# Kernel tuning notes

Measured on AMD Instinct MI355X. Metric: run time of the kernel, lower is better.

Reference implementation:

```python
import jax, jax.numpy as jnp
import numpy as np

B, S, D = 1, 2048, 2048
H, KVH, HD = 16, 8, 128
ROPE_THETA = 1e6
P_POW, C_SHIFT = 8, 7.0
MASK_VAL = -7.0  # = -c so masked bpmax base ~ scores only (finite under ^8)


def rotate_half(x):
    x1, x2 = jnp.split(x, 2, axis=-1)
    return jnp.concatenate([-x2, x1], axis=-1)


def setup_inputs() -> dict:
    key = jax.random.key(0)
    ks = jax.random.split(key, 10)
    hidden_states = jax.random.normal(ks[0], (B, S, D), dtype=jnp.float32)
    # RoPE tables (Qwen3-style, theta=1e6)
    inv_freq = 1.0 / (ROPE_THETA ** (jnp.arange(0, HD, 2, dtype=jnp.float32) / HD))
    freqs = jnp.arange(S, dtype=jnp.float32)[:, None] * inv_freq[None, :]
    emb = jnp.concatenate([freqs, freqs], axis=-1)  # [S, HD]
    cos = jnp.broadcast_to(jnp.cos(emb)[None], (B, S, HD)).astype(jnp.float32)
    sin = jnp.broadcast_to(jnp.sin(emb)[None], (B, S, HD)).astype(jnp.float32)
    sc = D ** -0.5
    q_proj_w = jax.random.normal(ks[1], (D, H * HD), dtype=jnp.float32) * sc
    k_proj_w = jax.random.normal(ks[2], (D, KVH * HD), dtype=jnp.float32) * sc
    v_proj_w = jax.random.normal(ks[3], (D, KVH * HD), dtype=jnp.float32) * sc
    o_proj_w = jax.random.normal(ks[4], (H * HD, D), dtype=jnp.float32) * (H * HD) ** -0.5
    q_norm_w = jnp.ones((HD,), dtype=jnp.float32)
    k_norm_w = jnp.ones((HD,), dtype=jnp.float32)
    # Stored RMSNorm denominators (rsqrt-like buffers from training), ~O(1)
    q_denom = 0.5 + jax.random.uniform(ks[5], (B, S, H, 1), dtype=jnp.float32)
    k_denom = 0.5 + jax.random.uniform(ks[6], (B, S, KVH, 1), dtype=jnp.float32)
    # Stored bpmax normalizer buffer rd (per-head, per-query-row)
    rd = 5.0 + 10.0 * jax.random.uniform(ks[7], (1, H, S, 1), dtype=jnp.float32)
    # Causal mask with MASK_VAL for masked positions (finite under bpmax)
    causal = jnp.tril(jnp.ones((S, S), dtype=bool))
    attention_mask = jnp.where(causal, 0.0, MASK_VAL)[None, None].astype(jnp.float32)
    return {
        'hidden_states': hidden_states, 'cos': cos, 'sin': sin,
        'q_proj_w': q_proj_w, 'k_proj_w': k_proj_w, 'v_proj_w': v_proj_w,
        'o_proj_w': o_proj_w, 'q_norm_w': q_norm_w, 'k_norm_w': k_norm_w,
        'q_denom': q_denom, 'k_denom': k_denom, 'rd': rd,
        'attention_mask': attention_mask,
    }


def reference(hidden_states, cos, sin, q_proj_w, k_proj_w, v_proj_w, o_proj_w,
              q_norm_w, k_norm_w, q_denom, k_denom, rd, attention_mask):
    b, s, d = hidden_states.shape
    hd = q_norm_w.shape[0]
    scaling = hd ** -0.5
    # Projections + per-head RMSNorm (eval path: stored denominator buffer)
    q = (hidden_states @ q_proj_w).reshape(b, s, -1, hd)
    q = (q_norm_w * (q * q_denom[:, :s])).transpose(0, 2, 1, 3)   # [B,H,S,hd]
    k = (hidden_states @ k_proj_w).reshape(b, s, -1, hd)
    k = (k_norm_w * (k * k_denom[:, :s])).transpose(0, 2, 1, 3)   # [B,KVH,S,hd]
    v = (hidden_states @ v_proj_w).reshape(b, s, -1, hd).transpose(0, 2, 1, 3)
    # RoPE
    cos_ = cos[:, None, :, :]
    sin_ = sin[:, None, :, :]
    q = q * cos_ + rotate_half(q) * sin_
    k = k * cos_ + rotate_half(k) * sin_
    # GQA: repeat kv heads
    groups = q.shape[1] // k.shape[1]
    k = jnp.repeat(k, groups, axis=1)
    v = jnp.repeat(v, groups, axis=1)
    # Scores + mask + bpmax power-law normalization (eval path)
    aw = jnp.einsum('bhqd,bhkd->bhqk', q, k) * scaling
    aw = aw + attention_mask[:, :, :, :s]
    aw = ((aw + C_SHIFT) / rd[:, :, :s, :]) ** P_POW
    # Attention output + output projection
    out = jnp.einsum('bhqk,bhkd->bhqd', aw, v)
    out = out.transpose(0, 2, 1, 3).reshape(b, s, -1)
    return out @ o_proj_w
```

## Files before the change

### kernel.cpp

```cpp
#include <hip/hip_runtime.h>
#include <cstdint>
#include <cstddef>


namespace {
constexpr int kS = 2048;
constexpr int kD = 2048;
constexpr int kH = 16;
constexpr int kKVH = 8;
constexpr int kHD = 128;
constexpr float kScale = 0.08838834764831845f;
constexpr size_t MB = 1u << 20;
}

using f32x4 = __attribute__((ext_vector_type(4))) float;
using bfrag = __attribute__((ext_vector_type(8))) short;
using float4v = __attribute__((ext_vector_type(4))) float;
using short4v = __attribute__((ext_vector_type(4))) short;

__device__ __forceinline__ unsigned short f2b(float f) {
  union { float f; unsigned u; } x; x.f = f;
  unsigned r = x.u + 0x7FFFu + ((x.u >> 16) & 1u);
  return (unsigned short)(r >> 16);
}

__device__ __forceinline__ float b2f(unsigned short u) {
  union { unsigned u; float f; } x; x.u = ((unsigned)u) << 16;
  return x.f;
}

__device__ __forceinline__ void gload_lds16(const void* g, void* l) {
  __builtin_amdgcn_global_load_lds(
      (const __attribute__((address_space(1))) unsigned*)g,
      (__attribute__((address_space(3))) unsigned*)l, 16, 0, 0);
}

__global__ __launch_bounds__(256) void qwen_cast_bf16(const float* __restrict__ in,
                                                      unsigned short* __restrict__ out,
                                                      int n4) {
  int i = blockIdx.x * 256 + threadIdx.x;
  if (i >= n4) return;
  float4v v = *(const float4v*)(in + (size_t)i * 4);
  short4v o;
  o[0] = (short)f2b(v[0]); o[1] = (short)f2b(v[1]);
  o[2] = (short)f2b(v[2]); o[3] = (short)f2b(v[3]);
  int i4 = i * 4;
  int row = i4 >> 11, col = i4 & 2047;
  int scol = col ^ ((row & 3) << 3);
  *(short4v*)(out + ((size_t)row << 11) + scol) = o;
}

__global__ __launch_bounds__(256) void qwen_tw(const float* __restrict__ in, int R, int C,
                                               unsigned short* __restrict__ out, int ldo) {
  __shared__ float t[64][65];
  int c0 = blockIdx.x * 64, r0 = blockIdx.y * 64;
  int tr = threadIdx.x >> 6, tc = threadIdx.x & 63;
#pragma unroll
  for (int p = 0; p < 16; ++p) {
    int i = p * 4 + tr;
    t[i][tc] = in[(size_t)(r0 + i) * C + c0 + tc];
  }
  __syncthreads();
#pragma unroll
  for (int p = 0; p < 16; ++p) {
    int i = p * 4 + tr;
    int orow = c0 + i;
    int ocol = r0 + tc;
    int scol = ocol ^ ((orow & 3) << 3);
    out[(size_t)orow * ldo + scol] = f2b(t[tc][i]);
  }
}

template <int BM, bool BF16OUT>
__global__ __launch_bounds__(256) void qwen_gemm_bt(const unsigned short* __restrict__ A,
                                                    const unsigned short* __restrict__ Bt,
                                                    void* __restrict__ Cv,
                                                    int M, int N, int K) {
  __shared__ unsigned short As[2][BM * 32];
  __shared__ unsigned short Bs[2][128 * 32];
  constexpr int MR = BM / 32;
  const int nwg = gridDim.x * gridDim.y;
  int lin = blockIdx.y * gridDim.x + blockIdx.x;
  if ((nwg & 7) == 0) { int qq = nwg >> 3; lin = (lin & 7) * qq + (lin >> 3); }
  const int bxx = lin % gridDim.x, byy = lin / gridDim.x;
  const int tid = threadIdx.x, lane = tid & 63, w = tid >> 6;
  const int wr = w >> 1, wc = w & 1;
  const int row0 = bxx * BM, col0 = byy * 128;
  f32x4 acc[MR][4] = {};
  const int koff = (lane >> 4) << 3;
  const int swz = (lane & 3) << 3;
  const int kread = koff ^ swz;
  const int rA = wr * (BM / 2) + (lane & 15);
  const int rB = wc * 64 + (lane & 15);

  auto stage = [&](int kt, int b) {
#pragma unroll
    for (int c = 0; c < BM / 64; ++c) {
      int off = (c * 256 + tid) * 16;
      int e = off >> 1;
      int r = e >> 5, cc = e & 31;
      gload_lds16(A + (size_t)(row0 + r) * K + kt + cc, (char*)(&As[b][0]) + off);
    }
#pragma unroll
    for (int c = 0; c < 2; ++c) {
      int off = (c * 256 + tid) * 16;
      int e = off >> 1;
      int r = e >> 5, cc = e & 31;
      gload_lds16(Bt + (size_t)(col0 + r) * K + kt + cc, (char*)(&Bs[b][0]) + off);
    }
  };

  const int nk = K >> 5;
  stage(0, 0);
  asm volatile("s_waitcnt vmcnt(0)" ::: "memory");
  __builtin_amdgcn_s_barrier();
  int buf = 0;
#pragma unroll 1
  for (int t = 0; t < nk; ++t) {
    if (t + 1 < nk) stage((t + 1) << 5, buf ^ 1);
    bfrag aF[MR], bF[4];
#pragma unroll
    for (int m = 0; m < MR; ++m)
      aF[m] = *(const bfrag*)(&As[buf][0] + (rA + m * 16) * 32 + kread);
#pragma unroll
    for (int n = 0; n < 4; ++n)
      bF[n] = *(const bfrag*)(&Bs[buf][0] + (rB + n * 16) * 32 + kread);
#pragma unroll
    for (int m = 0; m < MR; ++m)
#pragma unroll
      for (int n = 0; n < 4; ++n)
        acc[m][n] = __builtin_amdgcn_mfma_f32_16x16x32_bf16(aF[m], bF[n], acc[m][n], 0, 0, 0);
    asm volatile("s_waitcnt vmcnt(0)" ::: "memory");
    __builtin_amdgcn_s_barrier();
    buf ^= 1;
  }
  const int cr = (lane >> 4) << 2;
  const int cc2 = lane & 15;
#pragma unroll
  for (int m = 0; m < MR; ++m)
#pragma unroll
    for (int n = 0; n < 4; ++n) {
      int r = row0 + wr * (BM / 2) + m * 16 + cr;
      int c = col0 + wc * 64 + n * 16 + cc2;
#pragma unroll
      for (int j = 0; j < 4; ++j) {
        if constexpr (BF16OUT) {
          ((unsigned short*)Cv)[(size_t)(r + j) * N + c] = f2b(acc[m][n][j]);
        } else {
          ((float*)Cv)[(size_t)(r + j) * N + c] = acc[m][n][j];
        }
      }
    }
}

__global__ __launch_bounds__(256) void qwen_rope(const unsigned short* __restrict__ Cq16,
                                                 const float* __restrict__ cosb,
                                                 const float* __restrict__ sinb,
                                                 const float* __restrict__ qnw,
                                                 const float* __restrict__ knw,
                                                 const float* __restrict__ qden,
                                                 const float* __restrict__ kden,
                                                 unsigned short* __restrict__ Qb,
                                                 unsigned short* __restrict__ Kswz) {
  __shared__ unsigned short SMrow[4096];
  const int s = blockIdx.x;
  const int t = threadIdx.x;
  {
    const char* src = (const char*)(Cq16 + (size_t)s * 4096);
    gload_lds16(src + t * 16, (char*)SMrow + t * 16);
    gload_lds16(src + 4096 + t * 16, (char*)SMrow + 4096 + t * 16);
  }
  __syncthreads();
  const float* cs = cosb + (size_t)s * kHD;
  const float* sn = sinb + (size_t)s * kHD;
#pragma unroll
  for (int rep = 0; rep < 8; ++rep) {
    int idx = rep * 256 + t;
    int h = idx >> 7, d = idx & 127;
    float dn = qden[s * kH + h];
    float v = b2f(SMrow[idx]) * dn * qnw[d];
    float pv = b2f(SMrow[(h << 7) + (d ^ 64)]) * dn * qnw[d ^ 64];
    float rot = (d < 64) ? -pv : pv;
    Qb[((size_t)h * kS + s) * kHD + d] = f2b(v * cs[d] + rot * sn[d]);
  }
  const int kt = s >> 6, key = s & 63;
#pragma unroll
  for (int rep = 0; rep < 4; ++rep) {
    int idx = rep * 256 + t;
    int h = idx >> 7, d = idx & 127;
    float dn = kden[s * kKVH + h];
    float v = b2f(SMrow[2048 + idx]) * dn * knw[d];
    float pv = b2f(SMrow[2048 + (h << 7) + (d ^ 64)]) * dn * knw[d ^ 64];
    float rot = (d < 64) ? -pv : pv;
    size_t rowi = ((size_t)(h * 32 + kt) * 64 + key) * 128;
    Kswz[rowi + (d ^ ((key & 7) << 3))] = f2b(v * cs[d] + rot * sn[d]);
  }
}

__global__ __launch_bounds__(256) void qwen_vtr(const unsigned short* __restrict__ Cq16,
                                                unsigned short* __restrict__ Vswz) {
  __shared__ unsigned short t[64][66];
  int kvh = blockIdx.x, st = blockIdx.y, dt = blockIdx.z;
  int s0 = st * 64, d0 = dt * 64;
  int tr = threadIdx.x >> 6, tc = threadIdx.x & 63;
#pragma unroll
  for (int p = 0; p < 16; ++p) {
    int i = p * 4 + tr;
    t[i][tc] = Cq16[(size_t)(s0 + i) * 4096 + 3072 + (kvh << 7) + d0 + tc];
  }
  __syncthreads();
#pragma unroll
  for (int p = 0; p < 16; ++p) {
    int i = p * 4 + tr;
    int d = d0 + i;
    size_t rowi = ((size_t)(kvh * 32 + st) * 128 + d) * 64;
    Vswz[rowi + (tc ^ ((d & 15) << 2))] = t[tc][i];
  }
}

#define STAGE8(cc, bb)                                                 \
  do {                                                                 \
    const char* ks_ = Ksrc + ((size_t)(cc) << 14) + tid * 16;          \
    const char* vs_ = Vsrc + ((size_t)(cc) << 14) + tid * 16;          \
    char* kd_ = (char*)(&KV[bb][0]) + tid * 16;                        \
    char* vd_ = (char*)(&KV[2 + (bb)][0]) + tid * 16;                  \
    _Pragma("unroll") for (int it = 0; it < 4; ++it) {                 \
      gload_lds16(ks_ + it * 4096, kd_ + it * 4096);                   \
      gload_lds16(vs_ + it * 4096, vd_ + it * 4096);                   \
    }                                                                  \
  } while (0)

__global__ __launch_bounds__(256, 2) void qwen_attn(const unsigned short* __restrict__ Qb,
                                                    const unsigned short* __restrict__ Kswz,
                                                    const unsigned short* __restrict__ Vswz,
                                                    const float* __restrict__ rd,
                                                    unsigned short* __restrict__ AO) {
  __shared__ unsigned short KV[4][8192];
  const int bid = blockIdx.x;
  const int kvh = bid & 7;
  const int u = (bid >> 3) & 31;
  const int v = bid >> 8;
  const int h = kvh * 2 + (u & 1);
  const int j = u >> 1;
  const int qt = v ? j : (31 - j);
  const int q0 = qt * 64;
  const int nch = qt + 1;
  const int tid = threadIdx.x, lane = tid & 63, w = tid >> 6;
  const int l15 = lane & 15, g = lane >> 4;
  const int qw0 = q0 + w * 16;
  const int qlim = qw0 + l15;
  const int swzK = (l15 & 7) << 3;
  const int swzV = l15 << 2;

  bfrag qF[4];
#pragma unroll
  for (int dc = 0; dc < 4; ++dc)
    qF[dc] = *(const bfrag*)(Qb + ((size_t)h * kS + qw0 + l15) * kHD + dc * 32 + g * 8);
  const float inv = 1.0f / rd[(size_t)h * kS + qw0 + l15];

  const char* Ksrc = (const char*)Kswz + ((size_t)(kvh * 32) << 14);
  const char* Vsrc = (const char*)Vswz + ((size_t)(kvh * 32) << 14);

  f32x4 outa[8] = {};

  STAGE8(0, 0);
#pragma unroll 1
  for (int c = 0; c < nch; ++c) {
    const int b = c & 1;
    asm volatile("s_waitcnt vmcnt(0)" ::: "memory");
    __builtin_amdgcn_s_barrier();
    if (c + 1 < nch) STAGE8(c + 1, b ^ 1);
    __builtin_amdgcn_s_setprio(1);
    const unsigned short* Kbuf = &KV[b][0];
    const unsigned short* Vbuf = &KV[2 + b][0];
    f32x4 sc[4] = {};
#pragma unroll
    for (int t = 0; t < 4; ++t) {
      const unsigned short* kr = Kbuf + (t * 16 + l15) * 128;
#pragma unroll
      for (int dc = 0; dc < 4; ++dc) {
        bfrag kf = *(const bfrag*)(kr + ((dc * 32 + g * 8) ^ swzK));
        sc[t] = __builtin_amdgcn_mfma_f32_16x16x32_bf16(kf, qF[dc], sc[t], 0, 0, 0);
      }
    }
    const int kbase = c * 64;
    const bool full = (c < qt);
    union { bfrag f; unsigned u[4]; } pb[2];
#pragma unroll
    for (int t = 0; t < 4; ++t) {
      unsigned short bb[4];
#pragma unroll
      for (int rr = 0; rr < 4; ++rr) {
        float tt = sc[t][rr] * kScale;
        int key = kbase + t * 16 + g * 4 + rr;
        tt += (full || key <= qlim) ? 7.0f : 0.0f;
        float y = tt * inv;
        float y2 = y * y, y4 = y2 * y2;
        bb[rr] = f2b(y4 * y4);
      }
      pb[t >> 1].u[(t & 1) * 2 + 0] = (unsigned)bb[0] | ((unsigned)bb[1] << 16);
      pb[t >> 1].u[(t & 1) * 2 + 1] = (unsigned)bb[2] | ((unsigned)bb[3] << 16);
    }
#pragma unroll
    for (int dt = 0; dt < 8; ++dt) {
      const unsigned short* vr = Vbuf + (dt * 16 + l15) * 64;
#pragma unroll
      for (int pr = 0; pr < 2; ++pr) {
        union { bfrag f; short4v h4[2]; } va;
        va.h4[0] = *(const short4v*)(vr + ((pr * 32 + g * 4) ^ swzV));
        va.h4[1] = *(const short4v*)(vr + ((pr * 32 + 16 + g * 4) ^ swzV));
        outa[dt] = __builtin_amdgcn_mfma_f32_16x16x32_bf16(va.f, pb[pr].f, outa[dt], 0, 0, 0);
      }
    }
    __builtin_amdgcn_s_setprio(0);
  }
  {
    const int swzA = (l15 & 3) << 3;
#pragma unroll
    for (int dt = 0; dt < 8; ++dt) {
      short4v o;
      o[0] = (short)f2b(outa[dt][0]); o[1] = (short)f2b(outa[dt][1]);
      o[2] = (short)f2b(outa[dt][2]); o[3] = (short)f2b(outa[dt][3]);
      int col = h * 128 + dt * 16 + g * 4;
      *(short4v*)(AO + (size_t)(qw0 + l15) * kD + (col ^ swzA)) = o;
    }
  }
}

extern "C" void kernel_launch(void* const* d_in, const int* in_sizes, int n_in,
                              void* d_out, int out_size, void* d_ws, size_t ws_size,
                              hipStream_t stream) {
  (void)in_sizes; (void)n_in; (void)out_size; (void)ws_size;
  const float* hidden = (const float*)d_in[0];
  const float* cosb   = (const float*)d_in[1];
  const float* sinb   = (const float*)d_in[2];
  const float* qw     = (const float*)d_in[3];
  const float* kw     = (const float*)d_in[4];
  const float* vw     = (const float*)d_in[5];
  const float* ow     = (const float*)d_in[6];
  const float* qnw    = (const float*)d_in[7];
  const float* knw    = (const float*)d_in[8];
  const float* qden   = (const float*)d_in[9];
  const float* kden   = (const float*)d_in[10];
  const float* rd     = (const float*)d_in[11];
  float* out = (float*)d_out;

  char* ws = (char*)d_ws;
  unsigned short* hsb  = (unsigned short*)(ws + 0 * MB);
  unsigned short* Wt   = (unsigned short*)(ws + 8 * MB);
  unsigned short* Cq16 = (unsigned short*)(ws + 24 * MB);
  unsigned short* Qb   = (unsigned short*)(ws + 56 * MB);
  unsigned short* Kswz = (unsigned short*)(ws + 64 * MB);
  unsigned short* Vswz = (unsigned short*)(ws + 68 * MB);
  unsigned short* AO   = (unsigned short*)(ws + 72 * MB);
  unsigned short* Ot   = (unsigned short*)(ws + 80 * MB);

  qwen_cast_bf16<<<4096, 256, 0, stream>>>(hidden, hsb, 2048 * 2048 / 4);
  qwen_tw<<<dim3(32, 32), 256, 0, stream>>>(qw, 2048, 2048, Wt, 2048);
  qwen_tw<<<dim3(16, 32), 256, 0, stream>>>(kw, 2048, 1024, Wt + (size_t)2048 * 2048, 2048);
  qwen_tw<<<dim3(16, 32), 256, 0, stream>>>(vw, 2048, 1024, Wt + (size_t)3072 * 2048, 2048);
  qwen_tw<<<dim3(32, 32), 256, 0, stream>>>(ow, 2048, 2048, Ot, 2048);
  qwen_gemm_bt<128, true><<<dim3(16, 32), 256, 0, stream>>>(hsb, Wt, Cq16, 2048, 4096, 2048);
  qwen_rope<<<2048, 256, 0, stream>>>(Cq16, cosb, sinb, qnw, knw, qden, kden, Qb, Kswz);
  qwen_vtr<<<dim3(8, 32, 2), 256, 0, stream>>>(Cq16, Vswz);
  qwen_attn<<<512, 256, 0, stream>>>(Qb, Kswz, Vswz, rd, AO);
  qwen_gemm_bt<128, false><<<dim3(16, 16), 256, 0, stream>>>(AO, Ot, out, 2048, 2048, 2048);
}
```

Baseline: 168.4 us.

## Split attention over key chunks by parity with 128-row query tiles and reduction

```diff
diff --git a/kernel.cpp b/kernel.cpp
--- a/kernel.cpp
+++ b/kernel.cpp
@@ -234,72 +234,87 @@
                                                     const unsigned short* __restrict__ Kswz,
                                                     const unsigned short* __restrict__ Vswz,
                                                     const float* __restrict__ rd,
-                                                    unsigned short* __restrict__ AO) {
+                                                    float* __restrict__ Pacc) {
   __shared__ unsigned short KV[4][8192];
   const int bid = blockIdx.x;
   const int kvh = bid & 7;
-  const int u = (bid >> 3) & 31;
-  const int v = bid >> 8;
-  const int h = kvh * 2 + (u & 1);
-  const int j = u >> 1;
-  const int qt = v ? j : (31 - j);
-  const int q0 = qt * 64;
-  const int nch = qt + 1;
+  const int x = bid >> 3;
+  const int half = x >> 5;
+  const int x5 = x & 31;
+  const int hb = x5 >> 4;
+  const int t0 = x5 & 15;
+  const int qt = half ? t0 : (15 - t0);
+  const int parity = half;
+  const int h = kvh * 2 + hb;
+  const int q0 = qt * 128;
+  const int nlc = qt + 1;
   const int tid = threadIdx.x, lane = tid & 63, w = tid >> 6;
   const int l15 = lane & 15, g = lane >> 4;
-  const int qw0 = q0 + w * 16;
-  const int qlim = qw0 + l15;
+  const int qw0 = q0 + w * 32;
+  const int qlim0 = qw0 + l15;
+  const int qlim1 = qw0 + 16 + l15;
   const int swzK = (l15 & 7) << 3;
   const int swzV = l15 << 2;
 
-  bfrag qF[4];
-#pragma unroll
-  for (int dc = 0; dc < 4; ++dc)
-    qF[dc] = *(const bfrag*)(Qb + ((size_t)h * kS + qw0 + l15) * kHD + dc * 32 + g * 8);
-  const float inv = 1.0f / rd[(size_t)h * kS + qw0 + l15];
+  bfrag qF[2][4];
+#pragma unroll
+  for (int qs = 0; qs < 2; ++qs)
+#pragma unroll
+    for (int dc = 0; dc < 4; ++dc)
+      qF[qs][dc] = *(const bfrag*)(Qb + ((size_t)h * kS + qw0 + qs * 16 + l15) * kHD +
+                                   dc * 32 + g * 8);
+  const float inv[2] = {1.0f / rd[(size_t)h * kS + qlim0],
+                        1.0f / rd[(size_t)h * kS + qlim1]};
 
   const char* Ksrc = (const char*)Kswz + ((size_t)(kvh * 32) << 14);
   const char* Vsrc = (const char*)Vswz + ((size_t)(kvh * 32) << 14);
 
-  f32x4 outa[8] = {};
-
-  STAGE8(0, 0);
+  f32x4 outa[2][8] = {};
+
+  STAGE8(parity, 0);
 #pragma unroll 1
-  for (int c = 0; c < nch; ++c) {
-    const int b = c & 1;
+  for (int lc = 0; lc < nlc; ++lc) {
+    const int c = parity + 2 * lc;
+    const int b = lc & 1;
     asm volatile("s_waitcnt vmcnt(0)" ::: "memory");
     __builtin_amdgcn_s_barrier();
-    if (c + 1 < nch) STAGE8(c + 1, b ^ 1);
+    if (lc + 1 < nlc) STAGE8(c + 2, b ^ 1);
     __builtin_amdgcn_s_setprio(1);
     const unsigned short* Kbuf = &KV[b][0];
     const unsigned short* Vbuf = &KV[2 + b][0];
-    f32x4 sc[4] = {};
-#pragma unroll
-    for (int t = 0; t < 4; ++t) {
-      const unsigned short* kr = Kbuf + (t * 16 + l15) * 128;
+    f32x4 sc[2][4] = {};
+#pragma unroll
+    for (int t4 = 0; t4 < 4; ++t4) {
+      const unsigned short* kr = Kbuf + (t4 * 16 + l15) * 128;
 #pragma unroll
       for (int dc = 0; dc < 4; ++dc) {
         bfrag kf = *(const bfrag*)(kr + ((dc * 32 + g * 8) ^ swzK));
-        sc[t] = __builtin_amdgcn_mfma_f32_16x16x32_bf16(kf, qF[dc], sc[t], 0, 0, 0);
+        sc[0][t4] = __builtin_amdgcn_mfma_f32_16x16x32_bf16(kf, qF[0][dc], sc[0][t4], 0, 0, 0);
+        sc[1][t4] = __builtin_amdgcn_mfma_f32_16x16x32_bf16(kf, qF[1][dc], sc[1][t4], 0, 0, 0);
       }
     }
     const int kbase = c * 64;
-    const bool full = (c < qt);
-    union { bfrag f; unsigned u[4]; } pb[2];
-#pragma unroll
-    for (int t = 0; t < 4; ++t) {
-      unsigned short bb[4];
-#pragma unroll
-      for (int rr = 0; rr < 4; ++rr) {
-        float tt = sc[t][rr] * kScale;
-        int key = kbase + t * 16 + g * 4 + rr;
-        tt += (full || key <= qlim) ? 7.0f : 0.0f;
-        float y = tt * inv;
-        float y2 = y * y, y4 = y2 * y2;
-        bb[rr] = f2b(y4 * y4);
+    const bool full = (kbase + 63 <= qw0);
+    union { bfrag f; unsigned u[4]; } pb[2][2];
+#pragma unroll
+    for (int qs = 0; qs < 2; ++qs) {
+      const int ql = qs ? qlim1 : qlim0;
+      const float iv = inv[qs];
+#pragma unroll
+      for (int t4 = 0; t4 < 4; ++t4) {
+        unsigned short bb[4];
+#pragma unroll
+        for (int rr = 0; rr < 4; ++rr) {
+          float tt = sc[qs][t4][rr] * kScale;
+          int key = kbase + t4 * 16 + g * 4 + rr;
+          tt += (full || key <= ql) ? 7.0f : 0.0f;
+          float y = tt * iv;
+          float y2 = y * y, y4 = y2 * y2;
+          bb[rr] = f2b(y4 * y4);
+        }
+        pb[qs][t4 >> 1].u[(t4 & 1) * 2 + 0] = (unsigned)bb[0] | ((unsigned)bb[1] << 16);
+        pb[qs][t4 >> 1].u[(t4 & 1) * 2 + 1] = (unsigned)bb[2] | ((unsigned)bb[3] << 16);
       }
-      pb[t >> 1].u[(t & 1) * 2 + 0] = (unsigned)bb[0] | ((unsigned)bb[1] << 16);
-      pb[t >> 1].u[(t & 1) * 2 + 1] = (unsigned)bb[2] | ((unsigned)bb[3] << 16);
     }
 #pragma unroll
     for (int dt = 0; dt < 8; ++dt) {
@@ -309,21 +324,45 @@
         union { bfrag f; short4v h4[2]; } va;
         va.h4[0] = *(const short4v*)(vr + ((pr * 32 + g * 4) ^ swzV));
         va.h4[1] = *(const short4v*)(vr + ((pr * 32 + 16 + g * 4) ^ swzV));
-        outa[dt] = __builtin_amdgcn_mfma_f32_16x16x32_bf16(va.f, pb[pr].f, outa[dt], 0, 0, 0);
+        outa[0][dt] = __builtin_amdgcn_mfma_f32_16x16x32_bf16(va.f, pb[0][pr].f, outa[0][dt], 0, 0, 0);
+        outa[1][dt] = __builtin_amdgcn_mfma_f32_16x16x32_bf16(va.f, pb[1][pr].f, outa[1][dt], 0, 0, 0);
       }
     }
     __builtin_amdgcn_s_setprio(0);
   }
   {
-    const int swzA = (l15 & 3) << 3;
-#pragma unroll
-    for (int dt = 0; dt < 8; ++dt) {
-      short4v o;
-      o[0] = (short)f2b(outa[dt][0]); o[1] = (short)f2b(outa[dt][1]);
-      o[2] = (short)f2b(outa[dt][2]); o[3] = (short)f2b(outa[dt][3]);
-      int col = h * 128 + dt * 16 + g * 4;
-      *(short4v*)(AO + (size_t)(qw0 + l15) * kD + (col ^ swzA)) = o;
-    }
+    float* Po = Pacc + (((size_t)(h * 16 + qt) * 2 + parity) << 14);
+#pragma unroll
+    for (int qs = 0; qs < 2; ++qs) {
+      const int qrow = w * 32 + qs * 16 + l15;
+#pragma unroll
+      for (int dt = 0; dt < 8; ++dt) {
+        f32x4 v = outa[qs][dt];
+        *(f32x4*)(Po + qrow * 128 + dt * 16 + g * 4) = v;
+      }
+    }
+  }
+}
+
+__global__ __launch_bounds__(256) void qwen_ared(const float* __restrict__ Pacc,
+                                                 unsigned short* __restrict__ AO) {
+  const int unit = blockIdx.x;
+  const int h = unit >> 4, qt = unit & 15;
+  const float* P0 = Pacc + ((size_t)unit << 15);
+  const float* P1 = P0 + 16384;
+  const int t = threadIdx.x;
+#pragma unroll
+  for (int i = 0; i < 16; ++i) {
+    int idx = (i * 256 + t) * 4;
+    f32x4 a = *(const f32x4*)(P0 + idx);
+    f32x4 b = *(const f32x4*)(P1 + idx);
+    int qrow = idx >> 7, d = idx & 127;
+    int q = qt * 128 + qrow;
+    int col = h * 128 + d;
+    short4v o;
+    o[0] = (short)f2b(a[0] + b[0]); o[1] = (short)f2b(a[1] + b[1]);
+    o[2] = (short)f2b(a[2] + b[2]); o[3] = (short)f2b(a[3] + b[3]);
+    *(short4v*)(AO + (size_t)q * kD + (col ^ ((q & 3) << 3))) = o;
   }
 }
 
@@ -349,6 +388,7 @@
   unsigned short* hsb  = (unsigned short*)(ws + 0 * MB);
   unsigned short* Wt   = (unsigned short*)(ws + 8 * MB);
   unsigned short* Cq16 = (unsigned short*)(ws + 24 * MB);
+  float*          Pacc = (float*)(ws + 24 * MB);
   unsigned short* Qb   = (unsigned short*)(ws + 56 * MB);
   unsigned short* Kswz = (unsigned short*)(ws + 64 * MB);
   unsigned short* Vswz = (unsigned short*)(ws + 68 * MB);
@@ -363,6 +403,7 @@
   qwen_gemm_bt<128, true><<<dim3(16, 32), 256, 0, stream>>>(hsb, Wt, Cq16, 2048, 4096, 2048);
   qwen_rope<<<2048, 256, 0, stream>>>(Cq16, cosb, sinb, qnw, knw, qden, kden, Qb, Kswz);
   qwen_vtr<<<dim3(8, 32, 2), 256, 0, stream>>>(Cq16, Vswz);
-  qwen_attn<<<512, 256, 0, stream>>>(Qb, Kswz, Vswz, rd, AO);
-  qwen_gemm_bt<128, false><<<dim3(16, 16), 256, 0, stream>>>(AO, Ot, out, 2048, 2048, 2048);
-}
+  qwen_attn<<<512, 256, 0, stream>>>(Qb, Kswz, Vswz, rd, Pacc);
+  qwen_ared<<<256, 256, 0, stream>>>(Pacc, AO);
+  qwen_gemm_bt<64, false><<<dim3(32, 16), 256, 0, stream>>>(AO, Ot, out, 2048, 2048, 2048);
+}
```

After: 165.1 us. -2.0%, faster.
